# Optimization experiments

Measured on AMD Instinct MI355X. Metric: run time of the kernel, lower is better.

The kernel has to match this reference:

```python
import jax, jax.numpy as jnp
import numpy as np

KERNEL = 3  # unfold kernel size (stride 1, no padding)

def _unfold(x, k):
    # torch.nn.Unfold(kernel_size=k) equivalent: (B, C, H, W) -> (B, C*k*k, L)
    # channel ordering: index = c*k*k + i*k + j (channel outermost), matching torch.
    B, C, H, W = x.shape
    Ho, Wo = H - k + 1, W - k + 1
    cols = [x[:, :, i:i + Ho, j:j + Wo] for i in range(k) for j in range(k)]  # k*k x (B,C,Ho,Wo)
    u = jnp.stack(cols, axis=2)  # (B, C, k*k, Ho, Wo)
    return u.reshape(B, C * k * k, Ho * Wo)


def setup_inputs() -> dict:
    key = jax.random.key(0)
    k1, k2, k3, k4 = jax.random.split(key, 4)
    B, C, H, W = 512, 3, 64, 64
    M = 512            # num_neurons
    K = C * KERNEL * KERNEL   # input_dim = 27
    L = (H - KERNEL + 1) * (W - KERNEL + 1)  # 3844 patches
    O = 10             # output_dim
    x = jax.random.normal(k1, (B, C, H, W), dtype=jnp.float32)
    G = jax.random.normal(k2, (M, L), dtype=jnp.float32)
    # original inits v,w to zeros; use randn for a non-degenerate reference
    v = jax.random.normal(k3, (M, K, O), dtype=jnp.float32) * 0.02
    w = jax.random.normal(k4, (M, K, O), dtype=jnp.float32) * 0.02
    return {"x": x, "G": G, "v": v, "w": w}


def reference(x, G, v, w):
    # Faithful to:
    #   U = unfold(x)                         (B, K, L)
    #   t = einsum('mn,ikn->imnk', G, U)      (B, M, L, K)  <- never materialized here
    #   out = einsum('ijkl,jlm->im', t, v-w)  (B, O)
    # Reordered as two small contractions (same math, no huge intermediate):
    U = _unfold(x, KERNEL)                    # (B, K, L)
    A = jnp.einsum('bkn,mn->bmk', U, G)       # (B, M, K): contract over patches L
    p_diff = v - w                            # (M, K, O)
    out = jnp.einsum('bmk,mko->bo', A, p_diff)  # (B, O)
    return out
```

## Files before the change

kernel.cpp:

```cpp
#include <hip/hip_runtime.h>

#define M_NEUR 512
#define ODIM   10
#define HO     62
#define LDIM   3844
#define CHW    12288
#define BATCH  512
#define KO     270
#define NG     16
#define GS     17
#define PDS    24

__global__ __launch_bounds__(256)
void pd_kernel(const float* __restrict__ v, const float* __restrict__ w,
               float* __restrict__ pdY) {
    int idx = blockIdx.x * 256 + threadIdx.x;
    if (idx >= NG * M_NEUR * PDS) return;
    int g = idx / (M_NEUR * PDS);
    int r = idx - g * (M_NEUR * PDS);
    int m = r / PDS;
    int s = r - m * PDS;
    int ko = g * GS + s;
    float val = 0.f;
    if (s < GS && ko < KO) {
        int src = m * KO + ko;
        val = v[src] - w[src];
    }
    pdY[idx] = val;
}

__global__ __launch_bounds__(256)
void t_gemm_kernel(const float* __restrict__ G,
                   const float* __restrict__ pdY,
                   float* __restrict__ T) {
    const int id    = blockIdx.x;
    const int r     = id & 7;
    const int inner = id >> 3;
    const int g     = inner & 15;
    const int tile  = (inner >> 4) * 8 + r;
    if (tile >= 61) return;

    const int tid  = threadIdx.x;
    const int lane = tid & 63;
    const int mc   = tid >> 6;
    const int smc  = __builtin_amdgcn_readfirstlane(mc);

    const int n  = tile * 64 + lane;
    const int nc = (n < LDIM) ? n : (LDIM - 1);

    float acc[GS];
#pragma unroll
    for (int s = 0; s < GS; ++s) acc[s] = 0.f;

    const float* gp = G + (size_t)(smc * 128) * LDIM + nc;
    const float* pp = pdY + ((size_t)g * M_NEUR + smc * 128) * PDS;

#pragma unroll 4
    for (int mi = 0; mi < 128; ++mi) {
        float gv = gp[(size_t)mi * LDIM];
        const float* p = pp + mi * PDS;
#pragma unroll
        for (int s = 0; s < GS; ++s)
            acc[s] += gv * p[s];
    }

    __shared__ float red[3][GS][64];
    if (mc > 0) {
#pragma unroll
        for (int s = 0; s < GS; ++s) red[mc - 1][s][lane] = acc[s];
    }
    __syncthreads();
    if (mc == 0 && n < LDIM) {
#pragma unroll
        for (int s = 0; s < GS; ++s) {
            int ko = g * GS + s;
            if (ko < KO) {
                float sum = acc[s] + red[0][s][lane]
                          + red[1][s][lane] + red[2][s][lane];
                T[(size_t)ko * LDIM + n] = sum;
            }
        }
    }
}

__global__ __launch_bounds__(256)
void fold_kernel(const float* __restrict__ T, float* __restrict__ S) {
    int idx = blockIdx.x * 256 + threadIdx.x;
    int c = idx >> 12;
    int h = (idx >> 6) & 63;
    int w = idx & 63;

    float s[ODIM];
#pragma unroll
    for (int o = 0; o < ODIM; ++o) s[o] = 0.f;

    for (int i = 0; i < 3; ++i) {
        int pi = h - i;
        if ((unsigned)pi >= HO) continue;
        for (int j = 0; j < 3; ++j) {
            int pj = w - j;
            if ((unsigned)pj >= HO) continue;
            int kk = c * 9 + i * 3 + j;
            const float* tp = T + (size_t)kk * ODIM * LDIM + pi * HO + pj;
#pragma unroll
            for (int o = 0; o < ODIM; ++o) s[o] += tp[(size_t)o * LDIM];
        }
    }
#pragma unroll
    for (int o = 0; o < ODIM; ++o) S[o * CHW + idx] = s[o];
}

__global__ __launch_bounds__(256)
void out_gemm_kernel(const float* __restrict__ X,
                     const float* __restrict__ S,
                     float* __restrict__ out) {
    const int b0  = blockIdx.x * 2;
    const int tid = threadIdx.x;
    const int NV  = CHW / 4;
    const float4* X0 = reinterpret_cast<const float4*>(X) + (size_t)b0 * NV;
    const float4* X1 = X0 + NV;
    const float4* S4 = reinterpret_cast<const float4*>(S);

    float acc0[ODIM], acc1[ODIM];
#pragma unroll
    for (int o = 0; o < ODIM; ++o) { acc0[o] = 0.f; acc1[o] = 0.f; }

    for (int i = tid; i < NV; i += 256) {
        float4 a = X0[i];
        float4 b = X1[i];
#pragma unroll
        for (int o = 0; o < ODIM; ++o) {
            float4 sv = S4[(size_t)o * NV + i];
            acc0[o] += a.x * sv.x + a.y * sv.y + a.z * sv.z + a.w * sv.w;
            acc1[o] += b.x * sv.x + b.y * sv.y + b.z * sv.z + b.w * sv.w;
        }
    }

#pragma unroll
    for (int o = 0; o < ODIM; ++o) {
        float s0 = acc0[o], s1 = acc1[o];
        for (int off = 32; off > 0; off >>= 1) {
            s0 += __shfl_down(s0, off, 64);
            s1 += __shfl_down(s1, off, 64);
        }
        acc0[o] = s0; acc1[o] = s1;
    }

    __shared__ float red[4][2 * ODIM];
    int wave = tid >> 6;
    int lane = tid & 63;
    if (lane == 0) {
#pragma unroll
        for (int o = 0; o < ODIM; ++o) {
            red[wave][o] = acc0[o];
            red[wave][ODIM + o] = acc1[o];
        }
    }
    __syncthreads();
    if (tid < 2 * ODIM) {
        float tsum = red[0][tid] + red[1][tid] + red[2][tid] + red[3][tid];
        int bt = tid / ODIM;
        int o  = tid - bt * ODIM;
        out[(size_t)(b0 + bt) * ODIM + o] = tsum;
    }
}

extern "C" void kernel_launch(void* const* d_in, const int* in_sizes, int n_in,
                              void* d_out, int out_size, void* d_ws, size_t ws_size,
                              hipStream_t stream) {
    const float* x = (const float*)d_in[0];
    const float* G = (const float*)d_in[1];
    const float* v = (const float*)d_in[2];
    const float* w = (const float*)d_in[3];
    float* out = (float*)d_out;

    float* T   = (float*)d_ws;
    float* S   = T + (size_t)KO * LDIM;
    float* pdY = S + (size_t)ODIM * CHW;

    pd_kernel<<<(NG * M_NEUR * PDS + 255) / 256, 256, 0, stream>>>(v, w, pdY);

    t_gemm_kernel<<<1024, 256, 0, stream>>>(G, pdY, T);

    fold_kernel<<<CHW / 256, 256, 0, stream>>>(T, S);

    out_gemm_kernel<<<BATCH / 2, 256, 0, stream>>>(x, S, out);
}
```

Measured before the change: 51.82 us.

## Retile T GEMM into 4x4 register blocks with split-M partial outputs

The T = pd^T·G GEMM is restructured so each thread computes a 4x4 register tile using float4 loads of G and padded pd. Blocks now take one of four M-chunks and write partial sums to separate buffers instead of reducing through shared memory. The fold kernel sums the four partials and is parallelised over output dimension as well as pixels. This aims to raise arithmetic intensity and occupancy in the GEMM. In exchange it adds four times the T write traffic and more reads in the fold.

New measurement: 65.66 us. 1.27x slower.

```diff
diff --git a/kernel.cpp b/kernel.cpp
--- a/kernel.cpp
+++ b/kernel.cpp
@@ -7,107 +7,105 @@
 #define CHW    12288
 #define BATCH  512
 #define KO     270
-#define NG     16
-#define GS     17
-#define PDS    24
+#define KOP    272
+#define NPART  4
+#define TPSTR  ((size_t)KO * LDIM)
 
 __global__ __launch_bounds__(256)
 void pd_kernel(const float* __restrict__ v, const float* __restrict__ w,
-               float* __restrict__ pdY) {
+               float* __restrict__ pdP) {
     int idx = blockIdx.x * 256 + threadIdx.x;
-    if (idx >= NG * M_NEUR * PDS) return;
-    int g = idx / (M_NEUR * PDS);
-    int r = idx - g * (M_NEUR * PDS);
-    int m = r / PDS;
-    int s = r - m * PDS;
-    int ko = g * GS + s;
-    float val = 0.f;
-    if (s < GS && ko < KO) {
-        int src = m * KO + ko;
-        val = v[src] - w[src];
-    }
-    pdY[idx] = val;
+    if (idx >= M_NEUR * KOP) return;
+    int m  = idx / KOP;
+    int ko = idx - m * KOP;
+    pdP[idx] = (ko < KO) ? (v[m * KO + ko] - w[m * KO + ko]) : 0.f;
 }
 
-__global__ __launch_bounds__(256)
+__global__ __launch_bounds__(256, 4)
 void t_gemm_kernel(const float* __restrict__ G,
-                   const float* __restrict__ pdY,
-                   float* __restrict__ T) {
-    const int id    = blockIdx.x;
-    const int r     = id & 7;
-    const int inner = id >> 3;
-    const int g     = inner & 15;
-    const int tile  = (inner >> 4) * 8 + r;
-    if (tile >= 61) return;
+                   const float* __restrict__ pdP,
+                   float* __restrict__ Tp) {
+    const int bid  = blockIdx.x;
+    const int xcd  = bid & 7;
+    const int s    = bid >> 3;
+    const int q    = s / 17;
+    const int r    = s - q * 17;
+    const int grp  = xcd + 8 * q;
+    const int tile = grp >> 2;
+    const int mc   = grp & 3;
+    const int wv   = threadIdx.x >> 6;
+    const int lane = threadIdx.x & 63;
+    const int jt   = 4 * r + wv;
+    const int ko0  = jt * 4;
+    const int m0   = mc * 128;
 
-    const int tid  = threadIdx.x;
-    const int lane = tid & 63;
-    const int mc   = tid >> 6;
-    const int smc  = __builtin_amdgcn_readfirstlane(mc);
+    const int nb   = tile * 256 + lane * 4;
+    const bool nok = (nb < LDIM);
+    const int nbc  = nok ? nb : 0;
 
-    const int n  = tile * 64 + lane;
-    const int nc = (n < LDIM) ? n : (LDIM - 1);
+    const float4* Gp = reinterpret_cast<const float4*>(G + (size_t)m0 * LDIM + nbc);
+    const float4* Pp = reinterpret_cast<const float4*>(pdP + (size_t)m0 * KOP + ko0);
+    const int GS4 = LDIM / 4;
+    const int PS4 = KOP / 4;
 
-    float acc[GS];
+    float acc[4][4];
 #pragma unroll
-    for (int s = 0; s < GS; ++s) acc[s] = 0.f;
-
-    const float* gp = G + (size_t)(smc * 128) * LDIM + nc;
-    const float* pp = pdY + ((size_t)g * M_NEUR + smc * 128) * PDS;
+    for (int j = 0; j < 4; ++j)
+#pragma unroll
+        for (int nn = 0; nn < 4; ++nn) acc[j][nn] = 0.f;
 
 #pragma unroll 4
     for (int mi = 0; mi < 128; ++mi) {
-        float gv = gp[(size_t)mi * LDIM];
-        const float* p = pp + mi * PDS;
-#pragma unroll
-        for (int s = 0; s < GS; ++s)
-            acc[s] += gv * p[s];
+        float4 gv = Gp[(size_t)mi * GS4];
+        float4 pv = Pp[(size_t)mi * PS4];
+        acc[0][0] += pv.x * gv.x;  acc[0][1] += pv.x * gv.y;
+        acc[0][2] += pv.x * gv.z;  acc[0][3] += pv.x * gv.w;
+        acc[1][0] += pv.y * gv.x;  acc[1][1] += pv.y * gv.y;
+        acc[1][2] += pv.y * gv.z;  acc[1][3] += pv.y * gv.w;
+        acc[2][0] += pv.z * gv.x;  acc[2][1] += pv.z * gv.y;
+        acc[2][2] += pv.z * gv.z;  acc[2][3] += pv.z * gv.w;
+        acc[3][0] += pv.w * gv.x;  acc[3][1] += pv.w * gv.y;
+        acc[3][2] += pv.w * gv.z;  acc[3][3] += pv.w * gv.w;
     }
 
-    __shared__ float red[3][GS][64];
-    if (mc > 0) {
+    if (nok) {
+        float* tb = Tp + (size_t)mc * TPSTR;
 #pragma unroll
-        for (int s = 0; s < GS; ++s) red[mc - 1][s][lane] = acc[s];
-    }
-    __syncthreads();
-    if (mc == 0 && n < LDIM) {
-#pragma unroll
-        for (int s = 0; s < GS; ++s) {
-            int ko = g * GS + s;
+        for (int j = 0; j < 4; ++j) {
+            int ko = ko0 + j;
             if (ko < KO) {
-                float sum = acc[s] + red[0][s][lane]
-                          + red[1][s][lane] + red[2][s][lane];
-                T[(size_t)ko * LDIM + n] = sum;
+                float4 o4 = make_float4(acc[j][0], acc[j][1], acc[j][2], acc[j][3]);
+                *reinterpret_cast<float4*>(&tb[(size_t)ko * LDIM + nb]) = o4;
             }
         }
     }
 }
 
 __global__ __launch_bounds__(256)
-void fold_kernel(const float* __restrict__ T, float* __restrict__ S) {
+void fold_kernel(const float* __restrict__ Tp, float* __restrict__ S) {
     int idx = blockIdx.x * 256 + threadIdx.x;
-    int c = idx >> 12;
-    int h = (idx >> 6) & 63;
-    int w = idx & 63;
+    if (idx >= ODIM * CHW) return;
+    int o   = idx / CHW;
+    int chw = idx - o * CHW;
+    int c = chw >> 12;
+    int h = (chw >> 6) & 63;
+    int w = chw & 63;
 
-    float s[ODIM];
-#pragma unroll
-    for (int o = 0; o < ODIM; ++o) s[o] = 0.f;
-
+    float s = 0.f;
     for (int i = 0; i < 3; ++i) {
         int pi = h - i;
         if ((unsigned)pi >= HO) continue;
         for (int j = 0; j < 3; ++j) {
             int pj = w - j;
             if ((unsigned)pj >= HO) continue;
-            int kk = c * 9 + i * 3 + j;
-            const float* tp = T + (size_t)kk * ODIM * LDIM + pi * HO + pj;
+            int ko  = (c * 9 + i * 3 + j) * ODIM + o;
+            size_t off = (size_t)ko * LDIM + pi * HO + pj;
 #pragma unroll
-            for (int o = 0; o < ODIM; ++o) s[o] += tp[(size_t)o * LDIM];
+            for (int p = 0; p < NPART; ++p)
+                s += Tp[(size_t)p * TPSTR + off];
         }
     }
-#pragma unroll
-    for (int o = 0; o < ODIM; ++o) S[o * CHW + idx] = s[o];
+    S[idx] = s;
 }
 
 __global__ __launch_bounds__(256)
@@ -174,15 +172,15 @@
     const float* w = (const float*)d_in[3];
     float* out = (float*)d_out;
 
-    float* T   = (float*)d_ws;
-    float* S   = T + (size_t)KO * LDIM;
-    float* pdY = S + (size_t)ODIM * CHW;
+    float* Tp  = (float*)d_ws;
+    float* S   = Tp + (size_t)NPART * TPSTR;
+    float* pdP = S + (size_t)ODIM * CHW;
 
-    pd_kernel<<<(NG * M_NEUR * PDS + 255) / 256, 256, 0, stream>>>(v, w, pdY);
+    pd_kernel<<<(M_NEUR * KOP + 255) / 256, 256, 0, stream>>>(v, w, pdP);
 
-    t_gemm_kernel<<<1024, 256, 0, stream>>>(G, pdY, T);
+    t_gemm_kernel<<<1088, 256, 0, stream>>>(G, pdP, Tp);
 
-    fold_kernel<<<CHW / 256, 256, 0, stream>>>(T, S);
+    fold_kernel<<<(ODIM * CHW + 255) / 256, 256, 0, stream>>>(Tp, S);
 
     out_gemm_kernel<<<BATCH / 2, 256, 0, stream>>>(x, S, out);
 }
```
